# Performance work log

Hardware: AMD Instinct MI355X
Metric: run time of the kernel (lower is better)

## Reference

```python
import jax, jax.numpy as jnp
import numpy as np

N = 4096                 # num nodes
SP, GE, TE = 256, 8, 64  # modality input dims
E = 32                   # embed_dim == hidden_features == out_features
H = 2                    # num_heads
D3 = 3 * E               # combined dim = 96
NEG_SLOPE = 0.2


def setup_inputs() -> dict:
    key = jax.random.key(0)
    ks = iter(jax.random.split(key, 64))
    nrm = lambda shape, s=0.05: jax.random.normal(next(ks), shape, jnp.float32) * s
    inp = {
        "spatial": jax.random.normal(next(ks), (N, SP), jnp.float32),
        "genomic": jax.random.normal(next(ks), (N, GE), jnp.float32),
        "temporal": jax.random.normal(next(ks), (N, TE), jnp.float32),
        "adj_matrix": jax.random.randint(next(ks), (N, N), 0, 2, jnp.int32),
        # modality embedding MLPs (Linear + LayerNorm)
        "sp_w": nrm((SP, E)), "sp_b": jnp.zeros((E,)), "sp_lg": jnp.ones((E,)), "sp_lb": jnp.zeros((E,)),
        "ge_w": nrm((GE, E)), "ge_b": jnp.zeros((E,)), "ge_lg": jnp.ones((E,)), "ge_lb": jnp.zeros((E,)),
        "te_w": nrm((TE, E)), "te_b": jnp.zeros((E,)), "te_lg": jnp.ones((E,)), "te_lb": jnp.zeros((E,)),
        # GAT: W_shared [96 -> H*E], attention vector a [2E], out_proj [H*E -> E], LayerNorm(E)
        "gat_w": nrm((D3, H * E)), "gat_a": nrm((2 * E,)),
        "gat_ow": nrm((H * E, E)), "gat_ob": jnp.zeros((E,)),
        "gat_lg": jnp.ones((E,)), "gat_lb": jnp.zeros((E,)),
        # MultiheadAttention (embed 96): packed qkv in_proj and out_proj
        "mha_iw": nrm((D3, 3 * D3)), "mha_ib": jnp.zeros((3 * D3,)),
        "mha_ow": nrm((D3, D3)), "mha_ob": jnp.zeros((D3,)),
        # motor tower
        "m1_w": nrm((D3, 2 * E)), "m1_b": jnp.zeros((2 * E,)), "m1_lg": jnp.ones((2 * E,)), "m1_lb": jnp.zeros((2 * E,)),
        "m2_w": nrm((2 * E, E)), "m2_b": jnp.zeros((E,)), "m2_lg": jnp.ones((E,)), "m2_lb": jnp.zeros((E,)),
        "m3_w": nrm((E, 1)), "m3_b": jnp.zeros((1,)),
        # cognitive tower
        "c1_w": nrm((D3, 2 * E)), "c1_b": jnp.zeros((2 * E,)), "c1_lg": jnp.ones((2 * E,)), "c1_lb": jnp.zeros((2 * E,)),
        "c2_w": nrm((2 * E, E)), "c2_b": jnp.zeros((E,)), "c2_lg": jnp.ones((E,)), "c2_lb": jnp.zeros((E,)),
        "c3_w": nrm((E, 1)), "c3_b": jnp.zeros((1,)),
    }
    return inp


def _ln(x, g, b, eps=1e-5):
    m = x.mean(-1, keepdims=True)
    v = ((x - m) ** 2).mean(-1, keepdims=True)
    return (x - m) / jnp.sqrt(v + eps) * g + b


def _embed(x, w, b, lg, lb):
    return jax.nn.relu(_ln(x @ w + b, lg, lb))  # dropout is identity in eval


def _tower(x, w1, b1, lg1, lb1, w2, b2, lg2, lb2, w3, b3):
    h = jax.nn.relu(_ln(x @ w1 + b1, lg1, lb1))
    h = jax.nn.relu(_ln(h @ w2 + b2, lg2, lb2))
    return h @ w3 + b3


def reference(spatial, genomic, temporal, adj_matrix,
              sp_w, sp_b, sp_lg, sp_lb, ge_w, ge_b, ge_lg, ge_lb,
              te_w, te_b, te_lg, te_lb,
              gat_w, gat_a, gat_ow, gat_ob, gat_lg, gat_lb,
              mha_iw, mha_ib, mha_ow, mha_ob,
              m1_w, m1_b, m1_lg, m1_lb, m2_w, m2_b, m2_lg, m2_lb, m3_w, m3_b,
              c1_w, c1_b, c1_lg, c1_lb, c2_w, c2_b, c2_lg, c2_lb, c3_w, c3_b):
    n = spatial.shape[0]
    s_emb = _embed(spatial, sp_w, sp_b, sp_lg, sp_lb)
    g_emb = _embed(genomic, ge_w, ge_b, ge_lg, ge_lb)
    t_emb = _embed(temporal, te_w, te_b, te_lg, te_lb)
    combined = jnp.concatenate([s_emb, g_emb, t_emb], axis=-1)  # [N, 96]

    # --- TaskSpecificGAT ---
    h = (combined @ gat_w).reshape(n, H, E)  # [N, H, E]
    # e[i,j] = leaky_relu(a . [h_i ; h_j]) = leaky_relu((h @ a1)_i + (h @ a2)_j)
    a1, a2 = gat_a[:E], gat_a[E:]
    f1 = jnp.einsum('nhd,d->nh', h, a1)  # source term
    f2 = jnp.einsum('nhd,d->nh', h, a2)  # target term
    e = jax.nn.leaky_relu(f1[:, None, :] + f2[None, :, :], NEG_SLOPE)  # [N, N, H]
    e = jnp.where(adj_matrix[:, :, None] == 0, -jnp.inf, e)
    alpha = jax.nn.softmax(e, axis=1)  # softmax over neighbors j
    h_out = jnp.einsum('ijh,jhd->ihd', alpha, h).reshape(n, H * E)  # [N, 64]
    gat_out = _ln(h_out @ gat_ow + gat_ob, gat_lg, gat_lb)  # [N, 32]

    # gat_expanded = cat([gat_out]*3) -> [N, 96], attn over seq_len=1
    gx = jnp.tile(gat_out, (1, 3))
    # MHA with a single key/query: softmax over one key == 1, so output = out_proj(v)
    v = gx @ mha_iw[:, 2 * D3:] + mha_ib[2 * D3:]
    attn_out = v @ mha_ow + mha_ob

    final = attn_out + combined
    motor = _tower(final, m1_w, m1_b, m1_lg, m1_lb, m2_w, m2_b, m2_lg, m2_lb, m3_w, m3_b)
    cognitive = jax.nn.sigmoid(
        _tower(final, c1_w, c1_b, c1_lg, c1_lb, c2_w, c2_b, c2_lg, c2_lb, c3_w, c3_b))
    return (motor, cognitive)
```

## Files before the change

### kernel.cpp

```cpp
#include <hip/hip_runtime.h>
#include <math.h>

#define NN 4096
#define LOG2E 1.4426950408889634f

typedef short short8 __attribute__((ext_vector_type(8)));
typedef float f32x4 __attribute__((ext_vector_type(4)));

#define OFF_COMB   0u
#define OFF_F1     393216u
#define OFF_F2     401408u
#define OFF_W2     409616u
#define OFF_B2     412688u
#define OFF_HT     412800u
#define OFF_PART   543872u

__device__ inline unsigned short f2bf(float x) {
  unsigned u = __float_as_uint(x);
  unsigned r = u + 0x7FFFu + ((u >> 16) & 1u);
  return (unsigned short)(r >> 16);
}

__global__ __launch_bounds__(256) void k_comb(
    const float* __restrict__ spatial, const float* __restrict__ genomic,
    const float* __restrict__ temporal,
    const float* __restrict__ sp_w, const float* __restrict__ sp_b,
    const float* __restrict__ sp_lg, const float* __restrict__ sp_lb,
    const float* __restrict__ ge_w, const float* __restrict__ ge_b,
    const float* __restrict__ ge_lg, const float* __restrict__ ge_lb,
    const float* __restrict__ te_w, const float* __restrict__ te_b,
    const float* __restrict__ te_lg, const float* __restrict__ te_lb,
    const float* __restrict__ mha_iw, const float* __restrict__ mha_ib,
    const float* __restrict__ mha_ow, const float* __restrict__ mha_ob,
    float* __restrict__ ws)
{
  int t = threadIdx.x;
  int blk = blockIdx.x;

  if (blk >= 1536) {
    if (blk < 1548) {
      int idx = (blk - 1536) * 256 + t;
      int b = idx / 96, col = idx - b * 96;
      float acc = 0.f;
      for (int r = 0; r < 96; r++) {
        float fw = mha_iw[b * 288 + 192 + r]
                 + mha_iw[(b + 32) * 288 + 192 + r]
                 + mha_iw[(b + 64) * 288 + 192 + r];
        acc = fmaf(fw, mha_ow[r * 96 + col], acc);
      }
      ws[OFF_W2 + b * 96 + col] = acc;
    } else {
      if (t < 96) {
        float acc = mha_ob[t];
        for (int r = 0; r < 96; r++) acc = fmaf(mha_ib[192 + r], mha_ow[r * 96 + t], acc);
        ws[OFF_B2 + t] = acc;
      }
    }
    return;
  }

  int j = blk * 8 + (t >> 5);
  int grp = j >> 12;
  int row = j & 4095;
  int c = t & 31;

  float val;
  const float* lg;
  const float* lb;
  if (grp == 0) {
    const float* in = spatial + (size_t)row * 256;
    float a0 = 0.f, a1 = 0.f, a2 = 0.f, a3 = 0.f;
#pragma unroll 4
    for (int k = 0; k < 256; k += 4) {
      float4 x = *(const float4*)(in + k);
      a0 = fmaf(x.x, sp_w[(k)     * 32 + c], a0);
      a1 = fmaf(x.y, sp_w[(k + 1) * 32 + c], a1);
      a2 = fmaf(x.z, sp_w[(k + 2) * 32 + c], a2);
      a3 = fmaf(x.w, sp_w[(k + 3) * 32 + c], a3);
    }
    val = sp_b[c] + ((a0 + a1) + (a2 + a3));
    lg = sp_lg; lb = sp_lb;
  } else if (grp == 1) {
    const float* in = genomic + (size_t)row * 8;
    float4 x0 = *(const float4*)(in);
    float4 x1 = *(const float4*)(in + 4);
    float a0 = ge_b[c];
    a0 = fmaf(x0.x, ge_w[0 * 32 + c], a0);
    a0 = fmaf(x0.y, ge_w[1 * 32 + c], a0);
    a0 = fmaf(x0.z, ge_w[2 * 32 + c], a0);
    a0 = fmaf(x0.w, ge_w[3 * 32 + c], a0);
    a0 = fmaf(x1.x, ge_w[4 * 32 + c], a0);
    a0 = fmaf(x1.y, ge_w[5 * 32 + c], a0);
    a0 = fmaf(x1.z, ge_w[6 * 32 + c], a0);
    a0 = fmaf(x1.w, ge_w[7 * 32 + c], a0);
    val = a0;
    lg = ge_lg; lb = ge_lb;
  } else {
    const float* in = temporal + (size_t)row * 64;
    float a0 = 0.f, a1 = 0.f, a2 = 0.f, a3 = 0.f;
#pragma unroll 4
    for (int k = 0; k < 64; k += 4) {
      float4 x = *(const float4*)(in + k);
      a0 = fmaf(x.x, te_w[(k)     * 32 + c], a0);
      a1 = fmaf(x.y, te_w[(k + 1) * 32 + c], a1);
      a2 = fmaf(x.z, te_w[(k + 2) * 32 + c], a2);
      a3 = fmaf(x.w, te_w[(k + 3) * 32 + c], a3);
    }
    val = te_b[c] + ((a0 + a1) + (a2 + a3));
    lg = te_lg; lb = te_lb;
  }

  float s1 = val, s2 = val * val;
#pragma unroll
  for (int m = 1; m < 32; m <<= 1) {
    s1 += __shfl_xor(s1, m, 32);
    s2 += __shfl_xor(s2, m, 32);
  }
  float mean = s1 * (1.f / 32.f);
  float var  = s2 * (1.f / 32.f) - mean * mean;
  float y = fmaxf((val - mean) * rsqrtf(var + 1e-5f) * lg[c] + lb[c], 0.f);
  ws[OFF_COMB + (size_t)row * 96 + grp * 32 + c] = y;
}

__global__ __launch_bounds__(256) void k_proj(
    const float* __restrict__ gat_w, const float* __restrict__ gat_a,
    float* __restrict__ ws)
{
  __shared__ float h_s[4][64];
  int t = threadIdx.x;
  int w = t >> 6, d = t & 63;
  int row0 = blockIdx.x * 4;
  int row = row0 + w;

  const float* crow = ws + OFF_COMB + (size_t)row * 96;
  float a0 = 0.f, a1 = 0.f;
#pragma unroll 8
  for (int k = 0; k < 96; k += 2) {
    a0 = fmaf(crow[k],     gat_w[k * 64 + d],       a0);
    a1 = fmaf(crow[k + 1], gat_w[(k + 1) * 64 + d], a1);
  }
  float h = a0 + a1;

  int dc = d & 31;
  float p1 = h * gat_a[dc];
  float p2 = h * gat_a[32 + dc];
#pragma unroll
  for (int m = 1; m < 32; m <<= 1) {
    p1 += __shfl_xor(p1, m, 32);
    p2 += __shfl_xor(p2, m, 32);
  }
  if (dc == 0) {
    int head = d >> 5;
    ws[OFF_F1 + head * NN + row] = p1;
    ws[OFF_F2 + head * NN + row] = p2;
  }

  h_s[w][d] = h;
  __syncthreads();
  if (t < 64) {
    unsigned u0 = (unsigned)f2bf(h_s[0][t]) | ((unsigned)f2bf(h_s[1][t]) << 16);
    unsigned u1 = (unsigned)f2bf(h_s[2][t]) | ((unsigned)f2bf(h_s[3][t]) << 16);
    uint2 v; v.x = u0; v.y = u1;
    unsigned short* hT = (unsigned short*)(ws + OFF_HT);
    *(uint2*)(hT + (size_t)t * NN + row0) = v;
  }
}

template<int NSC>
__global__ __launch_bounds__(256) void k_gat4(
    const int* __restrict__ adj,
    const unsigned short* __restrict__ hT,
    const float* __restrict__ f1h,
    const float* __restrict__ f2h,
    float* __restrict__ part,
    float* __restrict__ lpart)
{
  constexpr int SLICE = NN / NSC;
  int t = threadIdx.x;
  int lane = t & 63, wv = t >> 6;
  int quad = lane >> 4, mrow = lane & 15;
  int ib = blockIdx.x * 64 + wv * 16;
  int i_lane = ib + mrow;
  int jb = blockIdx.y * SLICE;

  float f1v0 = f1h[i_lane];
  float f1v1 = f1h[NN + i_lane];

  f32x4 acc00 = {0.f, 0.f, 0.f, 0.f};
  f32x4 acc01 = {0.f, 0.f, 0.f, 0.f};
  f32x4 acc10 = {0.f, 0.f, 0.f, 0.f};
  f32x4 acc11 = {0.f, 0.f, 0.f, 0.f};
  float ls0 = 0.f, ls1 = 0.f;

  const int* adjRow = adj + (size_t)i_lane * NN;

#pragma unroll
  for (int ci = 0; ci < SLICE / 32; ci++) {
    int jq = jb + ci * 32 + quad * 8;
    int4 am0 = *(const int4*)(adjRow + jq);
    int4 am1 = *(const int4*)(adjRow + jq + 4);
    float4 fa = *(const float4*)(f2h + jq);
    float4 fb = *(const float4*)(f2h + jq + 4);
    float4 fc = *(const float4*)(f2h + NN + jq);
    float4 fd = *(const float4*)(f2h + NN + jq + 4);
    short8 b00 = *(const short8*)(hT + (size_t)(mrow)      * NN + jq);
    short8 b01 = *(const short8*)(hT + (size_t)(16 + mrow) * NN + jq);
    short8 b10 = *(const short8*)(hT + (size_t)(32 + mrow) * NN + jq);
    short8 b11 = *(const short8*)(hT + (size_t)(48 + mrow) * NN + jq);

    float f2a[8] = {fa.x, fa.y, fa.z, fa.w, fb.x, fb.y, fb.z, fb.w};
    float f2b[8] = {fc.x, fc.y, fc.z, fc.w, fd.x, fd.y, fd.z, fd.w};
    int   amv[8] = {am0.x, am0.y, am0.z, am0.w, am1.x, am1.y, am1.z, am1.w};

    union { short8 v; unsigned short u[8]; } a0, a1;
#pragma unroll
    for (int k = 0; k < 8; k++) {
      float e0 = f1v0 + f2a[k];
      float le0 = fmaxf(e0, 0.2f * e0);
      float w0 = __builtin_amdgcn_exp2f(le0 * LOG2E);
      float e1 = f1v1 + f2b[k];
      float le1 = fmaxf(e1, 0.2f * e1);
      float w1 = __builtin_amdgcn_exp2f(le1 * LOG2E);
      w0 = amv[k] ? w0 : 0.f;
      w1 = amv[k] ? w1 : 0.f;
      ls0 += w0; ls1 += w1;
      a0.u[k] = f2bf(w0);
      a1.u[k] = f2bf(w1);
    }
    acc00 = __builtin_amdgcn_mfma_f32_16x16x32_bf16(a0.v, b00, acc00, 0, 0, 0);
    acc01 = __builtin_amdgcn_mfma_f32_16x16x32_bf16(a0.v, b01, acc01, 0, 0, 0);
    acc10 = __builtin_amdgcn_mfma_f32_16x16x32_bf16(a1.v, b10, acc10, 0, 0, 0);
    acc11 = __builtin_amdgcn_mfma_f32_16x16x32_bf16(a1.v, b11, acc11, 0, 0, 0);
  }

  ls0 += __shfl_xor(ls0, 16); ls0 += __shfl_xor(ls0, 32);
  ls1 += __shfl_xor(ls1, 16); ls1 += __shfl_xor(ls1, 32);

  int slot = blockIdx.y;
#pragma unroll
  for (int r = 0; r < 4; r++) {
    int ig = ib + quad * 4 + r;
    float* p = part + (size_t)ig * (NSC * 64) + slot * 64;
    p[mrow]      = acc00[r];
    p[16 + mrow] = acc01[r];
    p[32 + mrow] = acc10[r];
    p[48 + mrow] = acc11[r];
  }
  if (lane < 16) {
    int ig = ib + lane;
    lpart[((size_t)ig * NSC + slot) * 2]     = ls0;
    lpart[((size_t)ig * NSC + slot) * 2 + 1] = ls1;
  }
}

template<int NSC>
__global__ __launch_bounds__(256) void k_post3(
    const float* __restrict__ gat_ow, const float* __restrict__ gat_ob,
    const float* __restrict__ gat_lg, const float* __restrict__ gat_lb,
    const float* __restrict__ m1_w, const float* __restrict__ m1_b,
    const float* __restrict__ m1_lg, const float* __restrict__ m1_lb,
    const float* __restrict__ m2_w, const float* __restrict__ m2_b,
    const float* __restrict__ m2_lg, const float* __restrict__ m2_lb,
    const float* __restrict__ m3_w, const float* __restrict__ m3_b,
    const float* __restrict__ c1_w, const float* __restrict__ c1_b,
    const float* __restrict__ c1_lg, const float* __restrict__ c1_lb,
    const float* __restrict__ c2_w, const float* __restrict__ c2_b,
    const float* __restrict__ c2_lg, const float* __restrict__ c2_lb,
    const float* __restrict__ c3_w, const float* __restrict__ c3_b,
    const float* __restrict__ part, const float* __restrict__ lpart,
    const float* __restrict__ comb, const float* __restrict__ W2,
    const float* __restrict__ B2,
    float* __restrict__ out)
{
  int t = threadIdx.x;
  int w = t >> 6, l = t & 63;
  int i = blockIdx.x * 4 + w;

  __shared__ float sh_h[4][64];
  __shared__ float sh_go[4][32];
  __shared__ float sh_fin[4][96];
  __shared__ float sh_t1[4][2][64];

  {
    const float* pr = part + (size_t)i * (NSC * 64);
    float a0 = 0.f, a1 = 0.f, a2 = 0.f, a3 = 0.f;
#pragma unroll
    for (int s = 0; s < NSC; s += 4) {
      a0 += pr[(s)     * 64 + l];
      a1 += pr[(s + 1) * 64 + l];
      a2 += pr[(s + 2) * 64 + l];
      a3 += pr[(s + 3) * 64 + l];
    }
    float a = (a0 + a1) + (a2 + a3);
    const float* lr = lpart + (size_t)i * NSC * 2;
    float l0 = 0.f, l1 = 0.f;
#pragma unroll
    for (int s = 0; s < NSC; s++) { l0 += lr[s * 2]; l1 += lr[s * 2 + 1]; }
    sh_h[w][l] = a / (l < 32 ? l0 : l1);
  }
  __syncthreads();

  if (l < 32) {
    float acc = gat_ob[l];
#pragma unroll 8
    for (int r = 0; r < 64; r++) acc = fmaf(sh_h[w][r], gat_ow[r * 32 + l], acc);
    float s1 = acc, s2 = acc * acc;
#pragma unroll
    for (int m = 1; m < 32; m <<= 1) {
      s1 += __shfl_xor(s1, m, 32);
      s2 += __shfl_xor(s2, m, 32);
    }
    float mean = s1 * (1.f / 32.f), var = s2 * (1.f / 32.f) - mean * mean;
    sh_go[w][l] = (acc - mean) * rsqrtf(var + 1e-5f) * gat_lg[l] + gat_lb[l];
  }
  __syncthreads();

  {
    float accA = B2[l];
#pragma unroll 8
    for (int d = 0; d < 32; d++) accA = fmaf(sh_go[w][d], W2[d * 96 + l], accA);
    sh_fin[w][l] = accA + comb[(size_t)i * 96 + l];
    if (l < 32) {
      float accB = B2[64 + l];
#pragma unroll 8
      for (int d = 0; d < 32; d++) accB = fmaf(sh_go[w][d], W2[d * 96 + 64 + l], accB);
      sh_fin[w][64 + l] = accB + comb[(size_t)i * 96 + 64 + l];
    }
  }
  __syncthreads();

  {
    float am = m1_b[l], ac = c1_b[l];
#pragma unroll 4
    for (int r = 0; r < 96; r++) {
      float f = sh_fin[w][r];
      am = fmaf(f, m1_w[r * 64 + l], am);
      ac = fmaf(f, c1_w[r * 64 + l], ac);
    }
    float s1 = am, s2 = am * am;
#pragma unroll
    for (int m = 1; m < 64; m <<= 1) { s1 += __shfl_xor(s1, m); s2 += __shfl_xor(s2, m); }
    float mean = s1 * (1.f / 64.f), var = s2 * (1.f / 64.f) - mean * mean;
    sh_t1[w][0][l] = fmaxf((am - mean) * rsqrtf(var + 1e-5f) * m1_lg[l] + m1_lb[l], 0.f);
    s1 = ac; s2 = ac * ac;
#pragma unroll
    for (int m = 1; m < 64; m <<= 1) { s1 += __shfl_xor(s1, m); s2 += __shfl_xor(s2, m); }
    mean = s1 * (1.f / 64.f); var = s2 * (1.f / 64.f) - mean * mean;
    sh_t1[w][1][l] = fmaxf((ac - mean) * rsqrtf(var + 1e-5f) * c1_lg[l] + c1_lb[l], 0.f);
  }
  __syncthreads();

  {
    int tw = l >> 5, c = l & 31;
    const float* w2  = tw ? c2_w  : m2_w;
    const float* b2  = tw ? c2_b  : m2_b;
    const float* lg2 = tw ? c2_lg : m2_lg;
    const float* lb2 = tw ? c2_lb : m2_lb;
    float a2 = b2[c];
#pragma unroll 4
    for (int r = 0; r < 64; r++) a2 = fmaf(sh_t1[w][tw][r], w2[r * 32 + c], a2);
    float u1 = a2, u2 = a2 * a2;
#pragma unroll
    for (int m = 1; m < 32; m <<= 1) {
      u1 += __shfl_xor(u1, m, 32);
      u2 += __shfl_xor(u2, m, 32);
    }
    float mean = u1 * (1.f / 32.f), var = u2 * (1.f / 32.f) - mean * mean;
    float y2 = fmaxf((a2 - mean) * rsqrtf(var + 1e-5f) * lg2[c] + lb2[c], 0.f);
    float p = y2 * (tw ? c3_w[c] : m3_w[c]);
#pragma unroll
    for (int m = 1; m < 32; m <<= 1) p += __shfl_xor(p, m, 32);
    if (c == 0) {
      float v = p + (tw ? c3_b[0] : m3_b[0]);
      if (tw) out[NN + i] = 1.f / (1.f + expf(-v));
      else    out[i] = v;
    }
  }
}

extern "C" void kernel_launch(void* const* d_in, const int* in_sizes, int n_in,
                              void* d_out, int out_size, void* d_ws, size_t ws_size,
                              hipStream_t stream) {
  (void)in_sizes; (void)n_in; (void)out_size;
  const float* spatial  = (const float*)d_in[0];
  const float* genomic  = (const float*)d_in[1];
  const float* temporal = (const float*)d_in[2];
  const int*   adj      = (const int*)d_in[3];
  const float* sp_w = (const float*)d_in[4];
  const float* sp_b = (const float*)d_in[5];
  const float* sp_lg = (const float*)d_in[6];
  const float* sp_lb = (const float*)d_in[7];
  const float* ge_w = (const float*)d_in[8];
  const float* ge_b = (const float*)d_in[9];
  const float* ge_lg = (const float*)d_in[10];
  const float* ge_lb = (const float*)d_in[11];
  const float* te_w = (const float*)d_in[12];
  const float* te_b = (const float*)d_in[13];
  const float* te_lg = (const float*)d_in[14];
  const float* te_lb = (const float*)d_in[15];
  const float* gat_w = (const float*)d_in[16];
  const float* gat_a = (const float*)d_in[17];
  const float* gat_ow = (const float*)d_in[18];
  const float* gat_ob = (const float*)d_in[19];
  const float* gat_lg = (const float*)d_in[20];
  const float* gat_lb = (const float*)d_in[21];
  const float* mha_iw = (const float*)d_in[22];
  const float* mha_ib = (const float*)d_in[23];
  const float* mha_ow = (const float*)d_in[24];
  const float* mha_ob = (const float*)d_in[25];
  const float* m1_w = (const float*)d_in[26];
  const float* m1_b = (const float*)d_in[27];
  const float* m1_lg = (const float*)d_in[28];
  const float* m1_lb = (const float*)d_in[29];
  const float* m2_w = (const float*)d_in[30];
  const float* m2_b = (const float*)d_in[31];
  const float* m2_lg = (const float*)d_in[32];
  const float* m2_lb = (const float*)d_in[33];
  const float* m3_w = (const float*)d_in[34];
  const float* m3_b = (const float*)d_in[35];
  const float* c1_w = (const float*)d_in[36];
  const float* c1_b = (const float*)d_in[37];
  const float* c1_lg = (const float*)d_in[38];
  const float* c1_lb = (const float*)d_in[39];
  const float* c2_w = (const float*)d_in[40];
  const float* c2_b = (const float*)d_in[41];
  const float* c2_lg = (const float*)d_in[42];
  const float* c2_lb = (const float*)d_in[43];
  const float* c3_w = (const float*)d_in[44];
  const float* c3_b = (const float*)d_in[45];

  float* ws  = (float*)d_ws;
  float* out = (float*)d_out;

  float* part  = ws + OFF_PART;

  k_comb<<<1549, 256, 0, stream>>>(spatial, genomic, temporal,
                                   sp_w, sp_b, sp_lg, sp_lb,
                                   ge_w, ge_b, ge_lg, ge_lb,
                                   te_w, te_b, te_lg, te_lb,
                                   mha_iw, mha_ib, mha_ow, mha_ob, ws);
  k_proj<<<NN / 4, 256, 0, stream>>>(gat_w, gat_a, ws);

  size_t need32 = (size_t)(OFF_PART + 32ul * NN * 64 + 32ul * NN * 2) * 4;
  size_t need16 = (size_t)(OFF_PART + 16ul * NN * 64 + 16ul * NN * 2) * 4;
  if (ws_size >= need32) {
    float* lpart = part + 32ul * NN * 64;
    dim3 g2(NN / 64, 32);
    k_gat4<32><<<g2, 256, 0, stream>>>(adj, (const unsigned short*)(ws + OFF_HT),
                                       ws + OFF_F1, ws + OFF_F2, part, lpart);
    k_post3<32><<<NN / 4, 256, 0, stream>>>(gat_ow, gat_ob, gat_lg, gat_lb,
                                            m1_w, m1_b, m1_lg, m1_lb,
                                            m2_w, m2_b, m2_lg, m2_lb,
                                            m3_w, m3_b,
                                            c1_w, c1_b, c1_lg, c1_lb,
                                            c2_w, c2_b, c2_lg, c2_lb,
                                            c3_w, c3_b,
                                            part, lpart, ws + OFF_COMB,
                                            ws + OFF_W2, ws + OFF_B2, out);
  } else if (ws_size >= need16) {
    float* lpart = part + 16ul * NN * 64;
    dim3 g2(NN / 64, 16);
    k_gat4<16><<<g2, 256, 0, stream>>>(adj, (const unsigned short*)(ws + OFF_HT),
                                       ws + OFF_F1, ws + OFF_F2, part, lpart);
    k_post3<16><<<NN / 4, 256, 0, stream>>>(gat_ow, gat_ob, gat_lg, gat_lb,
                                            m1_w, m1_b, m1_lg, m1_lb,
                                            m2_w, m2_b, m2_lg, m2_lb,
                                            m3_w, m3_b,
                                            c1_w, c1_b, c1_lg, c1_lb,
                                            c2_w, c2_b, c2_lg, c2_lb,
                                            c3_w, c3_b,
                                            part, lpart, ws + OFF_COMB,
                                            ws + OFF_W2, ws + OFF_B2, out);
  } else {
    float* lpart = part + 8ul * NN * 64;
    dim3 g2(NN / 64, 8);
    k_gat4<8><<<g2, 256, 0, stream>>>(adj, (const unsigned short*)(ws + OFF_HT),
                                      ws + OFF_F1, ws + OFF_F2, part, lpart);
    k_post3<8><<<NN / 4, 256, 0, stream>>>(gat_ow, gat_ob, gat_lg, gat_lb,
                                           m1_w, m1_b, m1_lg, m1_lb,
                                           m2_w, m2_b, m2_lg, m2_lb,
                                           m3_w, m3_b,
                                           c1_w, c1_b, c1_lg, c1_lb,
                                           c2_w, c2_b, c2_lg, c2_lb,
                                           c3_w, c3_b,
                                           part, lpart, ws + OFF_COMB,
                                           ws + OFF_W2, ws + OFF_B2, out);
  }
}
```

Before: 261.9 us.

## Pack adjacency into bitmasks in a prepass and consume bits in GAT kernel

Adds a prepass kernel that ballots the int32 adjacency matrix into 64-bit row masks. The GAT kernel then reads one 64-bit word per 64 neighbours instead of 64 ints, and each loop iteration covers 64 columns. The default split-K also drops from 32 to 16 slices. The full 64MB adjacency is still read once by the pack kernel, so the real saving is only the repeated mask traffic and the lighter inner loop, at the cost of an extra launch and a serial dependency.

```diff
diff --git a/kernel.cpp b/kernel.cpp
--- a/kernel.cpp
+++ b/kernel.cpp
@@ -13,12 +13,21 @@
 #define OFF_W2     409616u
 #define OFF_B2     412688u
 #define OFF_HT     412800u
-#define OFF_PART   543872u
+#define OFF_PACK   543872u
+#define OFF_PART   1068160u
 
 __device__ inline unsigned short f2bf(float x) {
   unsigned u = __float_as_uint(x);
   unsigned r = u + 0x7FFFu + ((u >> 16) & 1u);
   return (unsigned short)(r >> 16);
+}
+
+__global__ __launch_bounds__(256) void k_pack(
+    const int* __restrict__ adj, unsigned long long* __restrict__ pack)
+{
+  size_t t = (size_t)blockIdx.x * 256 + threadIdx.x;
+  unsigned long long m = __ballot(adj[t] != 0);
+  if ((threadIdx.x & 63) == 0) pack[t >> 6] = m;
 }
 
 __global__ __launch_bounds__(256) void k_comb(
@@ -167,8 +176,8 @@
 }
 
 template<int NSC>
-__global__ __launch_bounds__(256) void k_gat4(
-    const int* __restrict__ adj,
+__global__ __launch_bounds__(256) void k_gat5(
+    const unsigned long long* __restrict__ pack,
     const unsigned short* __restrict__ hT,
     const float* __restrict__ f1h,
     const float* __restrict__ f2h,
@@ -192,45 +201,81 @@
   f32x4 acc11 = {0.f, 0.f, 0.f, 0.f};
   float ls0 = 0.f, ls1 = 0.f;
 
-  const int* adjRow = adj + (size_t)i_lane * NN;
-
-#pragma unroll
-  for (int ci = 0; ci < SLICE / 32; ci++) {
-    int jq = jb + ci * 32 + quad * 8;
-    int4 am0 = *(const int4*)(adjRow + jq);
-    int4 am1 = *(const int4*)(adjRow + jq + 4);
-    float4 fa = *(const float4*)(f2h + jq);
-    float4 fb = *(const float4*)(f2h + jq + 4);
-    float4 fc = *(const float4*)(f2h + NN + jq);
-    float4 fd = *(const float4*)(f2h + NN + jq + 4);
-    short8 b00 = *(const short8*)(hT + (size_t)(mrow)      * NN + jq);
-    short8 b01 = *(const short8*)(hT + (size_t)(16 + mrow) * NN + jq);
-    short8 b10 = *(const short8*)(hT + (size_t)(32 + mrow) * NN + jq);
-    short8 b11 = *(const short8*)(hT + (size_t)(48 + mrow) * NN + jq);
-
-    float f2a[8] = {fa.x, fa.y, fa.z, fa.w, fb.x, fb.y, fb.z, fb.w};
-    float f2b[8] = {fc.x, fc.y, fc.z, fc.w, fd.x, fd.y, fd.z, fd.w};
-    int   amv[8] = {am0.x, am0.y, am0.z, am0.w, am1.x, am1.y, am1.z, am1.w};
-
-    union { short8 v; unsigned short u[8]; } a0, a1;
-#pragma unroll
-    for (int k = 0; k < 8; k++) {
-      float e0 = f1v0 + f2a[k];
-      float le0 = fmaxf(e0, 0.2f * e0);
-      float w0 = __builtin_amdgcn_exp2f(le0 * LOG2E);
-      float e1 = f1v1 + f2b[k];
-      float le1 = fmaxf(e1, 0.2f * e1);
-      float w1 = __builtin_amdgcn_exp2f(le1 * LOG2E);
-      w0 = amv[k] ? w0 : 0.f;
-      w1 = amv[k] ? w1 : 0.f;
-      ls0 += w0; ls1 += w1;
-      a0.u[k] = f2bf(w0);
-      a1.u[k] = f2bf(w1);
-    }
-    acc00 = __builtin_amdgcn_mfma_f32_16x16x32_bf16(a0.v, b00, acc00, 0, 0, 0);
-    acc01 = __builtin_amdgcn_mfma_f32_16x16x32_bf16(a0.v, b01, acc01, 0, 0, 0);
-    acc10 = __builtin_amdgcn_mfma_f32_16x16x32_bf16(a1.v, b10, acc10, 0, 0, 0);
-    acc11 = __builtin_amdgcn_mfma_f32_16x16x32_bf16(a1.v, b11, acc11, 0, 0, 0);
+  const unsigned long long* prow = pack + ((size_t)i_lane << 6);
+
+#pragma unroll
+  for (int ti = 0; ti < SLICE / 64; ti++) {
+    int jt = jb + ti * 64;
+    unsigned long long qm = prow[jt >> 6];
+    int jq0 = jt + quad * 8;
+    int jq1 = jq0 + 32;
+    float4 fa0 = *(const float4*)(f2h + jq0);
+    float4 fb0 = *(const float4*)(f2h + jq0 + 4);
+    float4 fa1 = *(const float4*)(f2h + jq1);
+    float4 fb1 = *(const float4*)(f2h + jq1 + 4);
+    float4 fc0 = *(const float4*)(f2h + NN + jq0);
+    float4 fd0 = *(const float4*)(f2h + NN + jq0 + 4);
+    float4 fc1 = *(const float4*)(f2h + NN + jq1);
+    float4 fd1 = *(const float4*)(f2h + NN + jq1 + 4);
+    short8 b00a = *(const short8*)(hT + (size_t)(mrow)      * NN + jq0);
+    short8 b01a = *(const short8*)(hT + (size_t)(16 + mrow) * NN + jq0);
+    short8 b10a = *(const short8*)(hT + (size_t)(32 + mrow) * NN + jq0);
+    short8 b11a = *(const short8*)(hT + (size_t)(48 + mrow) * NN + jq0);
+    short8 b00b = *(const short8*)(hT + (size_t)(mrow)      * NN + jq1);
+    short8 b01b = *(const short8*)(hT + (size_t)(16 + mrow) * NN + jq1);
+    short8 b10b = *(const short8*)(hT + (size_t)(32 + mrow) * NN + jq1);
+    short8 b11b = *(const short8*)(hT + (size_t)(48 + mrow) * NN + jq1);
+
+    {
+      float f2a[8] = {fa0.x, fa0.y, fa0.z, fa0.w, fb0.x, fb0.y, fb0.z, fb0.w};
+      float f2b[8] = {fc0.x, fc0.y, fc0.z, fc0.w, fd0.x, fd0.y, fd0.z, fd0.w};
+      unsigned mbits = (unsigned)(qm >> (quad * 8)) ;
+      union { short8 v; unsigned short u[8]; } a0, a1;
+#pragma unroll
+      for (int k = 0; k < 8; k++) {
+        float e0 = f1v0 + f2a[k];
+        float le0 = fmaxf(e0, 0.2f * e0);
+        float w0 = __builtin_amdgcn_exp2f(le0 * LOG2E);
+        float e1 = f1v1 + f2b[k];
+        float le1 = fmaxf(e1, 0.2f * e1);
+        float w1 = __builtin_amdgcn_exp2f(le1 * LOG2E);
+        bool on = (mbits >> k) & 1u;
+        w0 = on ? w0 : 0.f;
+        w1 = on ? w1 : 0.f;
+        ls0 += w0; ls1 += w1;
+        a0.u[k] = f2bf(w0);
+        a1.u[k] = f2bf(w1);
+      }
+      acc00 = __builtin_amdgcn_mfma_f32_16x16x32_bf16(a0.v, b00a, acc00, 0, 0, 0);
+      acc01 = __builtin_amdgcn_mfma_f32_16x16x32_bf16(a0.v, b01a, acc01, 0, 0, 0);
+      acc10 = __builtin_amdgcn_mfma_f32_16x16x32_bf16(a1.v, b10a, acc10, 0, 0, 0);
+      acc11 = __builtin_amdgcn_mfma_f32_16x16x32_bf16(a1.v, b11a, acc11, 0, 0, 0);
+    }
+    {
+      float f2a[8] = {fa1.x, fa1.y, fa1.z, fa1.w, fb1.x, fb1.y, fb1.z, fb1.w};
+      float f2b[8] = {fc1.x, fc1.y, fc1.z, fc1.w, fd1.x, fd1.y, fd1.z, fd1.w};
+      unsigned mbits = (unsigned)(qm >> (32 + quad * 8));
+      union { short8 v; unsigned short u[8]; } a0, a1;
+#pragma unroll
+      for (int k = 0; k < 8; k++) {
+        float e0 = f1v0 + f2a[k];
+        float le0 = fmaxf(e0, 0.2f * e0);
+        float w0 = __builtin_amdgcn_exp2f(le0 * LOG2E);
+        float e1 = f1v1 + f2b[k];
+        float le1 = fmaxf(e1, 0.2f * e1);
+        float w1 = __builtin_amdgcn_exp2f(le1 * LOG2E);
+        bool on = (mbits >> k) & 1u;
+        w0 = on ? w0 : 0.f;
+        w1 = on ? w1 : 0.f;
+        ls0 += w0; ls1 += w1;
+        a0.u[k] = f2bf(w0);
+        a1.u[k] = f2bf(w1);
+      }
+      acc00 = __builtin_amdgcn_mfma_f32_16x16x32_bf16(a0.v, b00b, acc00, 0, 0, 0);
+      acc01 = __builtin_amdgcn_mfma_f32_16x16x32_bf16(a0.v, b01b, acc01, 0, 0, 0);
+      acc10 = __builtin_amdgcn_mfma_f32_16x16x32_bf16(a1.v, b10b, acc10, 0, 0, 0);
+      acc11 = __builtin_amdgcn_mfma_f32_16x16x32_bf16(a1.v, b11b, acc11, 0, 0, 0);
+    }
   }
 
   ls0 += __shfl_xor(ls0, 16); ls0 += __shfl_xor(ls0, 32);
@@ -431,9 +476,9 @@
 
   float* ws  = (float*)d_ws;
   float* out = (float*)d_out;
-
-  float* part  = ws + OFF_PART;
-
+  float* part = ws + OFF_PART;
+
+  k_pack<<<(NN * NN) / 256, 256, 0, stream>>>(adj, (unsigned long long*)(ws + OFF_PACK));
   k_comb<<<1549, 256, 0, stream>>>(spatial, genomic, temporal,
                                    sp_w, sp_b, sp_lg, sp_lb,
                                    ge_w, ge_b, ge_lg, ge_lb,
@@ -441,26 +486,12 @@
                                    mha_iw, mha_ib, mha_ow, mha_ob, ws);
   k_proj<<<NN / 4, 256, 0, stream>>>(gat_w, gat_a, ws);
 
-  size_t need32 = (size_t)(OFF_PART + 32ul * NN * 64 + 32ul * NN * 2) * 4;
   size_t need16 = (size_t)(OFF_PART + 16ul * NN * 64 + 16ul * NN * 2) * 4;
-  if (ws_size >= need32) {
-    float* lpart = part + 32ul * NN * 64;
-    dim3 g2(NN / 64, 32);
-    k_gat4<32><<<g2, 256, 0, stream>>>(adj, (const unsigned short*)(ws + OFF_HT),
-                                       ws + OFF_F1, ws + OFF_F2, part, lpart);
-    k_post3<32><<<NN / 4, 256, 0, stream>>>(gat_ow, gat_ob, gat_lg, gat_lb,
-                                            m1_w, m1_b, m1_lg, m1_lb,
-                                            m2_w, m2_b, m2_lg, m2_lb,
-                                            m3_w, m3_b,
-                                            c1_w, c1_b, c1_lg, c1_lb,
-                                            c2_w, c2_b, c2_lg, c2_lb,
-                                            c3_w, c3_b,
-                                            part, lpart, ws + OFF_COMB,
-                                            ws + OFF_W2, ws + OFF_B2, out);
-  } else if (ws_size >= need16) {
+  if (ws_size >= need16) {
     float* lpart = part + 16ul * NN * 64;
     dim3 g2(NN / 64, 16);
-    k_gat4<16><<<g2, 256, 0, stream>>>(adj, (const unsigned short*)(ws + OFF_HT),
+    k_gat5<16><<<g2, 256, 0, stream>>>((const unsigned long long*)(ws + OFF_PACK),
+                                       (const unsigned short*)(ws + OFF_HT),
                                        ws + OFF_F1, ws + OFF_F2, part, lpart);
     k_post3<16><<<NN / 4, 256, 0, stream>>>(gat_ow, gat_ob, gat_lg, gat_lb,
                                             m1_w, m1_b, m1_lg, m1_lb,
@@ -474,7 +505,8 @@
   } else {
     float* lpart = part + 8ul * NN * 64;
     dim3 g2(NN / 64, 8);
-    k_gat4<8><<<g2, 256, 0, stream>>>(adj, (const unsigned short*)(ws + OFF_HT),
+    k_gat5<8><<<g2, 256, 0, stream>>>((const unsigned long long*)(ws + OFF_PACK),
+                                      (const unsigned short*)(ws + OFF_HT),
                                       ws + OFF_F1, ws + OFF_F2, part, lpart);
     k_post3<8><<<NN / 4, 256, 0, stream>>>(gat_ow, gat_ob, gat_lg, gat_lb,
                                            m1_w, m1_b, m1_lg, m1_lb,
```

After: 271.5 us. 3.7% more time.
